# Performance work log

Measured on AMD Instinct MI355X. Metric: run time of the kernel, lower is better.

## Reference

```python
import jax, jax.numpy as jnp
import numpy as np

N, IN_DIM, OUT_DIM, HEADS = 2048, 512, 512, 8
HEAD_DIM = OUT_DIM // HEADS
NEG_SLOPE = 0.2


def setup_inputs() -> dict:
    key = jax.random.key(0)
    k1, k2, k3, k4 = jax.random.split(key, 4)
    x = jax.random.normal(k1, (N, IN_DIM), dtype=jnp.float32)
    adj = jax.random.randint(k2, (N, N), 0, 2, dtype=jnp.int32)
    W = jax.random.normal(k3, (IN_DIM, OUT_DIM), dtype=jnp.float32) * 0.02
    a = jax.random.normal(k4, (2 * HEAD_DIM,), dtype=jnp.float32) * 0.02
    return {"x": x, "adj": adj, "W": W, "a": a}


def reference(x, adj, W, a):
    # Wh: (N, H, Dh)
    Wh = (x @ W).reshape(N, HEADS, HEAD_DIM)
    # a . concat(Wh_i, Wh_j) == (Wh_i . a_src) + (Wh_j . a_dst) -- exact decomposition,
    # avoids materializing the (N, N, H, 2*Dh) concat tensor.
    a_src, a_dst = a[:HEAD_DIM], a[HEAD_DIM:]
    s_i = jnp.einsum('nhd,d->nh', Wh, a_src)  # contribution of dest node i
    s_j = jnp.einsum('nhd,d->nh', Wh, a_dst)  # contribution of source node j
    e = jax.nn.leaky_relu(s_i[:, None, :] + s_j[None, :, :], negative_slope=NEG_SLOPE)  # (N, N, H)
    mask = (adj > 0)[:, :, None]
    e = jnp.where(mask, e, jnp.float32(-jnp.inf))
    alpha = jax.nn.softmax(e, axis=1)  # softmax over source nodes j
    # out[i,h,:] = sum_j alpha[i,j,h] * Wh[j,h,:]   (dropout is identity at eval)
    out = jnp.einsum('ijh,jhd->ihd', alpha, Wh)
    return out.reshape(N, OUT_DIM)
```

## Files before the change

### kernel.cpp

```cpp
#include <hip/hip_runtime.h>
#include <hip/hip_bf16.h>

#define NN 2048
#define KD 512
#define ODIM 512
#define NHEAD 8
#define HD 64
#define NEG 0.2f

typedef float f32x4 __attribute__((ext_vector_type(4)));
typedef short bf16x8 __attribute__((ext_vector_type(8)));
typedef short bf16x4 __attribute__((ext_vector_type(4)));
typedef unsigned long long u64;

__device__ __forceinline__ short tob(float f) {
  __hip_bfloat16 h = __float2bfloat16(f);
  return *reinterpret_cast<short*>(&h);
}

__global__ __launch_bounds__(256) void cast_wt(const float* __restrict__ W,
                                               __hip_bfloat16* __restrict__ WTb) {
  __shared__ float tile[64][68];
  const int t = threadIdx.x;
  const int k0 = blockIdx.x * 64, od0 = blockIdx.y * 64;
#pragma unroll
  for (int r = 0; r < 4; ++r) {
    const int flat = r * 256 + t;
    const int kk = flat >> 4, oq = (flat & 15) * 4;
    const float4 v = *(const float4*)&W[(size_t)(k0 + kk) * ODIM + od0 + oq];
    tile[kk][oq] = v.x;
    tile[kk][oq + 1] = v.y;
    tile[kk][oq + 2] = v.z;
    tile[kk][oq + 3] = v.w;
  }
  __syncthreads();
#pragma unroll
  for (int r = 0; r < 2; ++r) {
    const int flat = r * 256 + t;
    const int od = flat >> 3, kq = (flat & 7) * 8;
    bf16x8 o;
#pragma unroll
    for (int u = 0; u < 8; ++u) o[u] = tob(tile[kq + u][od]);
    *(bf16x8*)&WTb[(size_t)(od0 + od) * KD + k0 + kq] = o;
  }
}

__global__ __launch_bounds__(256) void pack_adj(const int* __restrict__ adj,
                                                unsigned short* __restrict__ bits) {
  const int T = blockIdx.x * 256 + threadIdx.x;
  const int row = T >> 7, g = T & 127;
  const int* p = adj + (size_t)row * NN + g * 16;
  unsigned int m = 0;
#pragma unroll
  for (int q = 0; q < 4; ++q) {
    const int4 v = *(const int4*)&p[q * 4];
    m |= (v.x > 0 ? 1u : 0u) << (q * 4);
    m |= (v.y > 0 ? 2u : 0u) << (q * 4);
    m |= (v.z > 0 ? 4u : 0u) << (q * 4);
    m |= (v.w > 0 ? 8u : 0u) << (q * 4);
  }
  bits[T] = (unsigned short)m;
}

__global__ __launch_bounds__(256) void gemm_fused(
    const float* __restrict__ X, const __hip_bfloat16* __restrict__ WTb,
    const float* __restrict__ a, short* __restrict__ WhF,
    float2* __restrict__ esrcp, unsigned int* __restrict__ edstp) {
  __shared__ short As[64][72];
  __shared__ short Bs[64][72];
  const int t = threadIdx.x;
  const int lane = t & 63, w = t >> 6;
  const int col = lane & 15, kgrp = lane >> 4;
  const int bm = blockIdx.x * 64;
  const int h = blockIdx.y;

  const int am = t >> 2, ak = (t & 3) * 16;
  const int bn = t >> 2, bk = (t & 3) * 16;

  float4 xa[4];
  bf16x8 wb[2];
#pragma unroll
  for (int q = 0; q < 4; ++q)
    xa[q] = *(const float4*)&X[(size_t)(bm + am) * KD + ak + q * 4];
#pragma unroll
  for (int q = 0; q < 2; ++q)
    wb[q] = *(const bf16x8*)&WTb[(size_t)(h * 64 + bn) * KD + bk + q * 8];

  f32x4 acc[4] = {};

  for (int k0 = 0; k0 < KD; k0 += 64) {
#pragma unroll
    for (int q = 0; q < 2; ++q) {
      bf16x8 o;
#pragma unroll
      for (int u = 0; u < 4; ++u) {
        o[u] = tob(((const float*)&xa[q * 2])[u]);
        o[u + 4] = tob(((const float*)&xa[q * 2 + 1])[u]);
      }
      *(bf16x8*)&As[am][ak + q * 8] = o;
      *(bf16x8*)&Bs[bn][bk + q * 8] = wb[q];
    }
    __syncthreads();
    if (k0 + 64 < KD) {
      const int k1 = k0 + 64;
#pragma unroll
      for (int q = 0; q < 4; ++q)
        xa[q] = *(const float4*)&X[(size_t)(bm + am) * KD + k1 + ak + q * 4];
#pragma unroll
      for (int q = 0; q < 2; ++q)
        wb[q] = *(const bf16x8*)&WTb[(size_t)(h * 64 + bn) * KD + k1 + bk + q * 8];
    }
#pragma unroll
    for (int ks = 0; ks < 2; ++ks) {
      const bf16x8 af = *(const bf16x8*)&As[w * 16 + col][ks * 32 + kgrp * 8];
#pragma unroll
      for (int nt = 0; nt < 4; ++nt) {
        const bf16x8 bf = *(const bf16x8*)&Bs[nt * 16 + col][ks * 32 + kgrp * 8];
        acc[nt] = __builtin_amdgcn_mfma_f32_16x16x32_bf16(af, bf, acc[nt], 0, 0, 0);
      }
    }
    __syncthreads();
  }

  float asv[4], adv[4];
#pragma unroll
  for (int nt = 0; nt < 4; ++nt) {
    asv[nt] = a[nt * 16 + col];
    adv[nt] = a[64 + nt * 16 + col];
  }
  float ps[4], pd[4];
#pragma unroll
  for (int r = 0; r < 4; ++r) {
    float s1 = 0.f, s2 = 0.f;
#pragma unroll
    for (int nt = 0; nt < 4; ++nt) {
      s1 += acc[nt][r] * asv[nt];
      s2 += acc[nt][r] * adv[nt];
    }
    ps[r] = s1;
    pd[r] = s2;
  }
#pragma unroll
  for (int off = 1; off <= 8; off <<= 1) {
#pragma unroll
    for (int r = 0; r < 4; ++r) {
      ps[r] += __shfl_xor(ps[r], off);
      pd[r] += __shfl_xor(pd[r], off);
    }
  }
  {
    const size_t tbase = ((size_t)h * 32 + blockIdx.x) * 4096;
    const int lp = ((w & 1) * 2 + (kgrp >> 1)) * 16 + col;
    const int u0 = (kgrp & 1) * 4;
    const int slot_ks = w >> 1;
#pragma unroll
    for (int nt = 0; nt < 4; ++nt) {
      bf16x4 o;
#pragma unroll
      for (int r = 0; r < 4; ++r) o[r] = tob(acc[nt][r]);
      *(bf16x4*)&WhF[tbase + (size_t)(nt * 2 + slot_ks) * 512 + lp * 8 + u0] = o;
    }
  }
  if (col == 0) {
    const int mbase = bm + w * 16 + kgrp * 4;
#pragma unroll
    for (int r = 0; r < 4; ++r) {
      const int n = mbase + r;
      esrcp[h * NN + n] = make_float2(__expf(ps[r]), __expf(NEG * ps[r]));
      const unsigned int lo = (unsigned int)(unsigned short)tob(__expf(pd[r]));
      const unsigned int hi = (unsigned int)(unsigned short)tob(__expf(NEG * pd[r]));
      edstp[h * NN + n] = (hi << 16) | lo;
    }
  }
}

__global__ __launch_bounds__(256, 2) void attn_mfma(
    const short* __restrict__ WhF, const unsigned char* __restrict__ adjbits,
    const float2* __restrict__ esrcp, const unsigned int* __restrict__ edstp,
    float* __restrict__ out) {
  __shared__ float accw[4][32][68];
  __shared__ float denw[4][32];

  const int t = threadIdx.x;
  const int lane = t & 63, w = t >> 6;
  const int col = lane & 15, kgrp = lane >> 4;
  const int h = blockIdx.y;
  const int i0 = blockIdx.x * 32;

  const float2 e0 = esrcp[h * NN + i0 + col];
  const float2 e1 = esrcp[h * NN + i0 + 16 + col];
  const float A0 = e0.x, C0 = e0.y, A1 = e1.x, C1 = e1.y;
  const unsigned char* ab0 = adjbits + (size_t)(i0 + col) * (NN / 8);
  const unsigned char* ab1 = adjbits + (size_t)(i0 + 16 + col) * (NN / 8);

  bf16x8 ones;
#pragma unroll
  for (int u = 0; u < 8; ++u) ones[u] = (short)0x3F80;

  f32x4 acc[2][4] = {};
  f32x4 accd[2] = {};

  const int jbase = w * 512;
  const short* tb = WhF + ((size_t)h * 32 + w * 8) * 4096;

  bf16x8 bc[8];
  uint4 bd[4];
  u64 aw0, aw1;
#pragma unroll
  for (int s = 0; s < 8; ++s) bc[s] = *(const bf16x8*)&tb[s * 512 + lane * 8];
#pragma unroll
  for (int ks = 0; ks < 2; ++ks) {
    const int jj = jbase + ks * 32 + kgrp * 8;
    bd[ks * 2] = *(const uint4*)&edstp[h * NN + jj];
    bd[ks * 2 + 1] = *(const uint4*)&edstp[h * NN + jj + 4];
  }
  aw0 = *(const u64*)(ab0 + (jbase >> 3));
  aw1 = *(const u64*)(ab1 + (jbase >> 3));

#pragma unroll
  for (int tt = 0; tt < 8; ++tt) {
    const int j0 = jbase + tt * 64;
    bf16x8 bn[8];
    uint4 bdn[4];
    u64 an0 = 0, an1 = 0;
    if (tt < 7) {
      const short* tbn = tb + (size_t)(tt + 1) * 4096;
      const int j1 = j0 + 64;
#pragma unroll
      for (int s = 0; s < 8; ++s)
        bn[s] = *(const bf16x8*)&tbn[s * 512 + lane * 8];
#pragma unroll
      for (int ks = 0; ks < 2; ++ks) {
        const int jj = j1 + ks * 32 + kgrp * 8;
        bdn[ks * 2] = *(const uint4*)&edstp[h * NN + jj];
        bdn[ks * 2 + 1] = *(const uint4*)&edstp[h * NN + jj + 4];
      }
      an0 = *(const u64*)(ab0 + (j1 >> 3));
      an1 = *(const u64*)(ab1 + (j1 >> 3));
    }

    bf16x8 af0[2], af1[2];
#pragma unroll
    for (int ks = 0; ks < 2; ++ks) {
      const unsigned int mb0 =
          (unsigned int)(aw0 >> ((ks * 4 + kgrp) * 8)) & 0xffu;
      const unsigned int mb1 =
          (unsigned int)(aw1 >> ((ks * 4 + kgrp) * 8)) & 0xffu;
      const uint4 q0 = bd[ks * 2], q1 = bd[ks * 2 + 1];
      const unsigned int uw[8] = {q0.x, q0.y, q0.z, q0.w,
                                  q1.x, q1.y, q1.z, q1.w};
#pragma unroll
      for (int u = 0; u < 8; ++u) {
        const float B = __uint_as_float(uw[u] << 16);
        const float D = __uint_as_float(uw[u] & 0xffff0000u);
        float p0 = fmaxf(A0 * B, C0 * D);
        float p1 = fmaxf(A1 * B, C1 * D);
        p0 = ((mb0 >> u) & 1u) ? p0 : 0.f;
        p1 = ((mb1 >> u) & 1u) ? p1 : 0.f;
        af0[ks][u] = tob(p0);
        af1[ks][u] = tob(p1);
      }
    }

    accd[0] = __builtin_amdgcn_mfma_f32_16x16x32_bf16(af0[0], ones, accd[0], 0, 0, 0);
    accd[0] = __builtin_amdgcn_mfma_f32_16x16x32_bf16(af0[1], ones, accd[0], 0, 0, 0);
    accd[1] = __builtin_amdgcn_mfma_f32_16x16x32_bf16(af1[0], ones, accd[1], 0, 0, 0);
    accd[1] = __builtin_amdgcn_mfma_f32_16x16x32_bf16(af1[1], ones, accd[1], 0, 0, 0);
#pragma unroll
    for (int nt = 0; nt < 4; ++nt) {
#pragma unroll
      for (int ks = 0; ks < 2; ++ks) {
        const bf16x8 b = bc[nt * 2 + ks];
        acc[0][nt] = __builtin_amdgcn_mfma_f32_16x16x32_bf16(af0[ks], b, acc[0][nt], 0, 0, 0);
        acc[1][nt] = __builtin_amdgcn_mfma_f32_16x16x32_bf16(af1[ks], b, acc[1][nt], 0, 0, 0);
      }
    }

    if (tt < 7) {
#pragma unroll
      for (int s = 0; s < 8; ++s) bc[s] = bn[s];
#pragma unroll
      for (int q = 0; q < 4; ++q) bd[q] = bdn[q];
      aw0 = an0;
      aw1 = an1;
    }
  }

#pragma unroll
  for (int mt = 0; mt < 2; ++mt)
#pragma unroll
    for (int nt = 0; nt < 4; ++nt)
#pragma unroll
      for (int r = 0; r < 4; ++r)
        accw[w][mt * 16 + kgrp * 4 + r][nt * 16 + col] = acc[mt][nt][r];
  if (col == 0) {
#pragma unroll
    for (int mt = 0; mt < 2; ++mt)
#pragma unroll
      for (int r = 0; r < 4; ++r)
        denw[w][mt * 16 + kgrp * 4 + r] = accd[mt][r];
  }
  __syncthreads();

  const int d = t & 63, mq = t >> 6;
#pragma unroll
  for (int rr = 0; rr < 8; ++rr) {
    const int m = rr * 4 + mq;
    float v = accw[0][m][d] + accw[1][m][d] + accw[2][m][d] + accw[3][m][d];
    float dd = denw[0][m] + denw[1][m] + denw[2][m] + denw[3][m];
    out[(size_t)(i0 + m) * ODIM + h * HD + d] = v / dd;
  }
}

extern "C" void kernel_launch(void* const* d_in, const int* in_sizes, int n_in,
                              void* d_out, int out_size, void* d_ws,
                              size_t ws_size, hipStream_t stream) {
  const float* x = (const float*)d_in[0];
  const int* adj = (const int*)d_in[1];
  const float* W = (const float*)d_in[2];
  const float* a = (const float*)d_in[3];
  float* out = (float*)d_out;

  char* ws = (char*)d_ws;
  short* WhF = (short*)ws;
  __hip_bfloat16* WTb = (__hip_bfloat16*)(ws + (2 << 20));
  unsigned short* bits =
      (unsigned short*)(ws + (2 << 20) + (512 << 10));
  float2* esrcp = (float2*)(ws + (3 << 20));
  unsigned int* edstp = (unsigned int*)(ws + (3 << 20) + (128 << 10));

  cast_wt<<<dim3(8, 8), 256, 0, stream>>>(W, WTb);
  pack_adj<<<1024, 256, 0, stream>>>(adj, bits);
  gemm_fused<<<dim3(32, 8), 256, 0, stream>>>(x, WTb, a, WhF, esrcp, edstp);
  attn_mfma<<<dim3(64, 8), 256, 0, stream>>>(
      WhF, (const unsigned char*)bits, esrcp, edstp, out);
}
```

Baseline: 39.78 us.

## Share WhF tiles across wave pairs via LDS async loads; merge prep kernels

Merges the W cast/transpose and adjacency bit-packing kernels into one launch to save a kernel launch. The attention kernel grows to 512 threads with 64 destination rows per block. Pairs of waves now share each source-node tile of Wh: each wave loads half of it straight into double-buffered LDS with global_load_lds, which halves global traffic for Wh per row processed. The cost is a block barrier every iteration, 66KB of dynamic shared memory, and half as many blocks in the grid.

```diff
diff --git a/kernel.cpp b/kernel.cpp
--- a/kernel.cpp
+++ b/kernel.cpp
@@ -12,17 +12,43 @@
 typedef short bf16x8 __attribute__((ext_vector_type(8)));
 typedef short bf16x4 __attribute__((ext_vector_type(4)));
 typedef unsigned long long u64;
+typedef unsigned int u32;
 
 __device__ __forceinline__ short tob(float f) {
   __hip_bfloat16 h = __float2bfloat16(f);
   return *reinterpret_cast<short*>(&h);
 }
 
-__global__ __launch_bounds__(256) void cast_wt(const float* __restrict__ W,
-                                               __hip_bfloat16* __restrict__ WTb) {
+__device__ __forceinline__ void gl_lds16(const void* g, void* l) {
+  __builtin_amdgcn_global_load_lds(
+      (const __attribute__((address_space(1))) u32*)g,
+      (__attribute__((address_space(3))) u32*)l, 16, 0, 0);
+}
+
+__global__ __launch_bounds__(256) void prep(const float* __restrict__ W,
+                                            const int* __restrict__ adj,
+                                            __hip_bfloat16* __restrict__ WTb,
+                                            unsigned short* __restrict__ bits) {
+  const int b = blockIdx.x;
+  const int t = threadIdx.x;
+  if (b >= 64) {
+    const int T = (b - 64) * 256 + t;
+    const int row = T >> 7, g = T & 127;
+    const int* p = adj + (size_t)row * NN + g * 16;
+    u32 m = 0;
+#pragma unroll
+    for (int q = 0; q < 4; ++q) {
+      const int4 v = *(const int4*)&p[q * 4];
+      m |= (v.x > 0 ? 1u : 0u) << (q * 4);
+      m |= (v.y > 0 ? 2u : 0u) << (q * 4);
+      m |= (v.z > 0 ? 4u : 0u) << (q * 4);
+      m |= (v.w > 0 ? 8u : 0u) << (q * 4);
+    }
+    bits[T] = (unsigned short)m;
+    return;
+  }
   __shared__ float tile[64][68];
-  const int t = threadIdx.x;
-  const int k0 = blockIdx.x * 64, od0 = blockIdx.y * 64;
+  const int k0 = (b & 7) * 64, od0 = (b >> 3) * 64;
 #pragma unroll
   for (int r = 0; r < 4; ++r) {
     const int flat = r * 256 + t;
@@ -45,27 +71,10 @@
   }
 }
 
-__global__ __launch_bounds__(256) void pack_adj(const int* __restrict__ adj,
-                                                unsigned short* __restrict__ bits) {
-  const int T = blockIdx.x * 256 + threadIdx.x;
-  const int row = T >> 7, g = T & 127;
-  const int* p = adj + (size_t)row * NN + g * 16;
-  unsigned int m = 0;
-#pragma unroll
-  for (int q = 0; q < 4; ++q) {
-    const int4 v = *(const int4*)&p[q * 4];
-    m |= (v.x > 0 ? 1u : 0u) << (q * 4);
-    m |= (v.y > 0 ? 2u : 0u) << (q * 4);
-    m |= (v.z > 0 ? 4u : 0u) << (q * 4);
-    m |= (v.w > 0 ? 8u : 0u) << (q * 4);
-  }
-  bits[T] = (unsigned short)m;
-}
-
 __global__ __launch_bounds__(256) void gemm_fused(
     const float* __restrict__ X, const __hip_bfloat16* __restrict__ WTb,
     const float* __restrict__ a, short* __restrict__ WhF,
-    float2* __restrict__ esrcp, unsigned int* __restrict__ edstp) {
+    float2* __restrict__ esrcp, u32* __restrict__ edstp) {
   __shared__ short As[64][72];
   __shared__ short Bs[64][72];
   const int t = threadIdx.x;
@@ -167,31 +176,36 @@
     for (int r = 0; r < 4; ++r) {
       const int n = mbase + r;
       esrcp[h * NN + n] = make_float2(__expf(ps[r]), __expf(NEG * ps[r]));
-      const unsigned int lo = (unsigned int)(unsigned short)tob(__expf(pd[r]));
-      const unsigned int hi = (unsigned int)(unsigned short)tob(__expf(NEG * pd[r]));
+      const u32 lo = (u32)(unsigned short)tob(__expf(pd[r]));
+      const u32 hi = (u32)(unsigned short)tob(__expf(NEG * pd[r]));
       edstp[h * NN + n] = (hi << 16) | lo;
     }
   }
 }
 
-__global__ __launch_bounds__(256, 2) void attn_mfma(
+__global__ __launch_bounds__(512) void attn_mfma(
     const short* __restrict__ WhF, const unsigned char* __restrict__ adjbits,
-    const float2* __restrict__ esrcp, const unsigned int* __restrict__ edstp,
+    const float2* __restrict__ esrcp, const u32* __restrict__ edstp,
     float* __restrict__ out) {
-  __shared__ float accw[4][32][68];
-  __shared__ float denw[4][32];
+  extern __shared__ __align__(16) char smem[];
+  short* stage = (short*)smem;
+  float* red = (float*)smem;
 
   const int t = threadIdx.x;
-  const int lane = t & 63, w = t >> 6;
+  const int lane = t & 63;
+  const int wid = t >> 6;
+  const int jq = wid >> 1;
+  const int mh = wid & 1;
   const int col = lane & 15, kgrp = lane >> 4;
   const int h = blockIdx.y;
-  const int i0 = blockIdx.x * 32;
-
-  const float2 e0 = esrcp[h * NN + i0 + col];
-  const float2 e1 = esrcp[h * NN + i0 + 16 + col];
+  const int i0 = blockIdx.x * 64;
+  const int ib = i0 + mh * 32;
+
+  const float2 e0 = esrcp[h * NN + ib + col];
+  const float2 e1 = esrcp[h * NN + ib + 16 + col];
   const float A0 = e0.x, C0 = e0.y, A1 = e1.x, C1 = e1.y;
-  const unsigned char* ab0 = adjbits + (size_t)(i0 + col) * (NN / 8);
-  const unsigned char* ab1 = adjbits + (size_t)(i0 + 16 + col) * (NN / 8);
+  const unsigned char* ab0 = adjbits + (size_t)(ib + col) * (NN / 8);
+  const unsigned char* ab1 = adjbits + (size_t)(ib + 16 + col) * (NN / 8);
 
   bf16x8 ones;
 #pragma unroll
@@ -200,115 +214,121 @@
   f32x4 acc[2][4] = {};
   f32x4 accd[2] = {};
 
-  const int jbase = w * 512;
-  const short* tb = WhF + ((size_t)h * 32 + w * 8) * 4096;
-
-  bf16x8 bc[8];
-  uint4 bd[4];
+  const short* tb = WhF + ((size_t)h * 32 + jq * 8) * 4096;
+  const int jb = jq * 512;
+  short* st0 = stage + (size_t)jq * (2 * 8 * 512);
+
+#pragma unroll
+  for (int s = 0; s < 4; ++s) {
+    const int slot = mh * 4 + s;
+    gl_lds16(tb + slot * 512 + lane * 8, st0 + slot * 512);
+  }
+  uint4 bd0, bd1, bd2, bd3;
   u64 aw0, aw1;
-#pragma unroll
-  for (int s = 0; s < 8; ++s) bc[s] = *(const bf16x8*)&tb[s * 512 + lane * 8];
-#pragma unroll
-  for (int ks = 0; ks < 2; ++ks) {
-    const int jj = jbase + ks * 32 + kgrp * 8;
-    bd[ks * 2] = *(const uint4*)&edstp[h * NN + jj];
-    bd[ks * 2 + 1] = *(const uint4*)&edstp[h * NN + jj + 4];
-  }
-  aw0 = *(const u64*)(ab0 + (jbase >> 3));
-  aw1 = *(const u64*)(ab1 + (jbase >> 3));
+  {
+    const int jj0 = jb + kgrp * 8;
+    bd0 = *(const uint4*)&edstp[h * NN + jj0];
+    bd1 = *(const uint4*)&edstp[h * NN + jj0 + 4];
+    bd2 = *(const uint4*)&edstp[h * NN + jj0 + 32];
+    bd3 = *(const uint4*)&edstp[h * NN + jj0 + 36];
+    aw0 = *(const u64*)(ab0 + (jb >> 3));
+    aw1 = *(const u64*)(ab1 + (jb >> 3));
+  }
+  __syncthreads();
 
 #pragma unroll
   for (int tt = 0; tt < 8; ++tt) {
-    const int j0 = jbase + tt * 64;
-    bf16x8 bn[8];
-    uint4 bdn[4];
+    short* scur = st0 + (tt & 1) * (8 * 512);
+    short* snxt = st0 + ((tt + 1) & 1) * (8 * 512);
+    if (tt < 7) {
+      const short* g = tb + (size_t)(tt + 1) * 4096;
+#pragma unroll
+      for (int s = 0; s < 4; ++s) {
+        const int slot = mh * 4 + s;
+        gl_lds16(g + slot * 512 + lane * 8, snxt + slot * 512);
+      }
+    }
+    uint4 bn0, bn1, bn2, bn3;
     u64 an0 = 0, an1 = 0;
     if (tt < 7) {
-      const short* tbn = tb + (size_t)(tt + 1) * 4096;
-      const int j1 = j0 + 64;
-#pragma unroll
-      for (int s = 0; s < 8; ++s)
-        bn[s] = *(const bf16x8*)&tbn[s * 512 + lane * 8];
-#pragma unroll
-      for (int ks = 0; ks < 2; ++ks) {
-        const int jj = j1 + ks * 32 + kgrp * 8;
-        bdn[ks * 2] = *(const uint4*)&edstp[h * NN + jj];
-        bdn[ks * 2 + 1] = *(const uint4*)&edstp[h * NN + jj + 4];
-      }
+      const int j1 = jb + (tt + 1) * 64;
+      const int jj1 = j1 + kgrp * 8;
+      bn0 = *(const uint4*)&edstp[h * NN + jj1];
+      bn1 = *(const uint4*)&edstp[h * NN + jj1 + 4];
+      bn2 = *(const uint4*)&edstp[h * NN + jj1 + 32];
+      bn3 = *(const uint4*)&edstp[h * NN + jj1 + 36];
       an0 = *(const u64*)(ab0 + (j1 >> 3));
       an1 = *(const u64*)(ab1 + (j1 >> 3));
     }
-
     bf16x8 af0[2], af1[2];
 #pragma unroll
     for (int ks = 0; ks < 2; ++ks) {
-      const unsigned int mb0 =
-          (unsigned int)(aw0 >> ((ks * 4 + kgrp) * 8)) & 0xffu;
-      const unsigned int mb1 =
-          (unsigned int)(aw1 >> ((ks * 4 + kgrp) * 8)) & 0xffu;
-      const uint4 q0 = bd[ks * 2], q1 = bd[ks * 2 + 1];
-      const unsigned int uw[8] = {q0.x, q0.y, q0.z, q0.w,
-                                  q1.x, q1.y, q1.z, q1.w};
-#pragma unroll
-      for (int u = 0; u < 8; ++u) {
-        const float B = __uint_as_float(uw[u] << 16);
-        const float D = __uint_as_float(uw[u] & 0xffff0000u);
+      const u32 mb0 = (u32)(aw0 >> ((ks * 4 + kgrp) * 8)) & 0xffu;
+      const u32 mb1 = (u32)(aw1 >> ((ks * 4 + kgrp) * 8)) & 0xffu;
+      const uint4 q0 = ks ? bd2 : bd0;
+      const uint4 q1 = ks ? bd3 : bd1;
+      const u32 uw[8] = {q0.x, q0.y, q0.z, q0.w, q1.x, q1.y, q1.z, q1.w};
+#pragma unroll
+      for (int u2 = 0; u2 < 8; ++u2) {
+        const float B = __uint_as_float(uw[u2] << 16);
+        const float D = __uint_as_float(uw[u2] & 0xffff0000u);
         float p0 = fmaxf(A0 * B, C0 * D);
         float p1 = fmaxf(A1 * B, C1 * D);
-        p0 = ((mb0 >> u) & 1u) ? p0 : 0.f;
-        p1 = ((mb1 >> u) & 1u) ? p1 : 0.f;
-        af0[ks][u] = tob(p0);
-        af1[ks][u] = tob(p1);
+        p0 = ((mb0 >> u2) & 1u) ? p0 : 0.f;
+        p1 = ((mb1 >> u2) & 1u) ? p1 : 0.f;
+        af0[ks][u2] = tob(p0);
+        af1[ks][u2] = tob(p1);
       }
     }
-
     accd[0] = __builtin_amdgcn_mfma_f32_16x16x32_bf16(af0[0], ones, accd[0], 0, 0, 0);
     accd[0] = __builtin_amdgcn_mfma_f32_16x16x32_bf16(af0[1], ones, accd[0], 0, 0, 0);
     accd[1] = __builtin_amdgcn_mfma_f32_16x16x32_bf16(af1[0], ones, accd[1], 0, 0, 0);
     accd[1] = __builtin_amdgcn_mfma_f32_16x16x32_bf16(af1[1], ones, accd[1], 0, 0, 0);
 #pragma unroll
     for (int nt = 0; nt < 4; ++nt) {
-#pragma unroll
-      for (int ks = 0; ks < 2; ++ks) {
-        const bf16x8 b = bc[nt * 2 + ks];
-        acc[0][nt] = __builtin_amdgcn_mfma_f32_16x16x32_bf16(af0[ks], b, acc[0][nt], 0, 0, 0);
-        acc[1][nt] = __builtin_amdgcn_mfma_f32_16x16x32_bf16(af1[ks], b, acc[1][nt], 0, 0, 0);
-      }
-    }
-
+      const bf16x8 b0 = *(const bf16x8*)&scur[(nt * 2 + 0) * 512 + lane * 8];
+      const bf16x8 b1 = *(const bf16x8*)&scur[(nt * 2 + 1) * 512 + lane * 8];
+      acc[0][nt] = __builtin_amdgcn_mfma_f32_16x16x32_bf16(af0[0], b0, acc[0][nt], 0, 0, 0);
+      acc[1][nt] = __builtin_amdgcn_mfma_f32_16x16x32_bf16(af1[0], b0, acc[1][nt], 0, 0, 0);
+      acc[0][nt] = __builtin_amdgcn_mfma_f32_16x16x32_bf16(af0[1], b1, acc[0][nt], 0, 0, 0);
+      acc[1][nt] = __builtin_amdgcn_mfma_f32_16x16x32_bf16(af1[1], b1, acc[1][nt], 0, 0, 0);
+    }
+    __syncthreads();
     if (tt < 7) {
-#pragma unroll
-      for (int s = 0; s < 8; ++s) bc[s] = bn[s];
-#pragma unroll
-      for (int q = 0; q < 4; ++q) bd[q] = bdn[q];
-      aw0 = an0;
-      aw1 = an1;
-    }
-  }
-
-#pragma unroll
-  for (int mt = 0; mt < 2; ++mt)
+      bd0 = bn0; bd1 = bn1; bd2 = bn2; bd3 = bn3;
+      aw0 = an0; aw1 = an1;
+    }
+  }
+
+  float* rw = red + (size_t)(mh * 4 + jq) * 32 * 66;
+#pragma unroll
+  for (int mt = 0; mt < 2; ++mt) {
 #pragma unroll
     for (int nt = 0; nt < 4; ++nt)
 #pragma unroll
       for (int r = 0; r < 4; ++r)
-        accw[w][mt * 16 + kgrp * 4 + r][nt * 16 + col] = acc[mt][nt][r];
-  if (col == 0) {
-#pragma unroll
-    for (int mt = 0; mt < 2; ++mt)
+        rw[(mt * 16 + kgrp * 4 + r) * 66 + nt * 16 + col] = acc[mt][nt][r];
+    if (col == 0) {
 #pragma unroll
       for (int r = 0; r < 4; ++r)
-        denw[w][mt * 16 + kgrp * 4 + r] = accd[mt][r];
+        rw[(mt * 16 + kgrp * 4 + r) * 66 + 64] = accd[mt][r];
+    }
   }
   __syncthreads();
 
-  const int d = t & 63, mq = t >> 6;
+  const int d = t & 63, rl = t >> 6;
 #pragma unroll
   for (int rr = 0; rr < 8; ++rr) {
-    const int m = rr * 4 + mq;
-    float v = accw[0][m][d] + accw[1][m][d] + accw[2][m][d] + accw[3][m][d];
-    float dd = denw[0][m] + denw[1][m] + denw[2][m] + denw[3][m];
-    out[(size_t)(i0 + m) * ODIM + h * HD + d] = v / dd;
+    const int row = rr * 8 + rl;
+    const int m2 = row >> 5, r32 = row & 31;
+    const float* rb = red + (size_t)(m2 * 4) * 32 * 66;
+    float v = 0.f, dd = 0.f;
+#pragma unroll
+    for (int q = 0; q < 4; ++q) {
+      v += rb[(q * 32 + r32) * 66 + d];
+      dd += rb[(q * 32 + r32) * 66 + 64];
+    }
+    out[(size_t)(i0 + row) * ODIM + h * HD + d] = v / dd;
   }
 }
 
@@ -327,11 +347,10 @@
   unsigned short* bits =
       (unsigned short*)(ws + (2 << 20) + (512 << 10));
   float2* esrcp = (float2*)(ws + (3 << 20));
-  unsigned int* edstp = (unsigned int*)(ws + (3 << 20) + (128 << 10));
-
-  cast_wt<<<dim3(8, 8), 256, 0, stream>>>(W, WTb);
-  pack_adj<<<1024, 256, 0, stream>>>(adj, bits);
+  u32* edstp = (u32*)(ws + (3 << 20) + (128 << 10));
+
+  prep<<<1088, 256, 0, stream>>>(W, adj, WTb, bits);
   gemm_fused<<<dim3(32, 8), 256, 0, stream>>>(x, WTb, a, WhF, esrcp, edstp);
-  attn_mfma<<<dim3(64, 8), 256, 0, stream>>>(
+  attn_mfma<<<dim3(32, 8), 512, 67584, stream>>>(
       WhF, (const unsigned char*)bits, esrcp, edstp, out);
 }
```

Result: faster. 36.72 us (-7.7%).
